# Optimization experiments

Measured on AMD Instinct MI355X. Metric: run time of the kernel, lower is better.

## Reference

```python
import jax, jax.numpy as jnp
import numpy as np

EPS = 1e-12


def setup_inputs() -> dict:
    key = jax.random.key(0)
    k1, k2, k3, k4 = jax.random.split(key, 4)
    N, H, W, D, K = 64, 32, 32, 512, 64
    x = jax.random.normal(k1, (N, H, W, D), dtype=jnp.float32)
    W_assign = jax.random.normal(k2, (D, K), dtype=jnp.float32) * 0.05  # 1x1 conv kernel
    b_assign = jax.random.normal(k3, (K,), dtype=jnp.float32) * 0.05
    C = jax.random.normal(k4, (D, K), dtype=jnp.float32) * 0.05  # cluster centers
    return {"x": x, "W_assign": W_assign, "b_assign": b_assign, "C": C}


def _l2norm(v, axis):
    return v / jnp.sqrt(jnp.sum(v * v, axis=axis, keepdims=True) + EPS)


def reference(x, W_assign, b_assign, C):
    # 1x1 conv = matmul over channel dim: [N,H,W,D] @ [D,K] -> [N,H,W,K]
    s = jnp.einsum('nhwd,dk->nhwk', x, W_assign) + b_assign
    a = jax.nn.softmax(s, axis=-1)                       # soft assignment over K
    # VLAD: v[n,d,k] = sum_hw a[n,h,w,k] * (x[n,h,w,d] + C[d,k])
    # reformulated as two small contractions (no [N,H,W,D,K] intermediate):
    v = jnp.einsum('nhwd,nhwk->ndk', x, a)               # feature-weighted sums
    a_sum = jnp.sum(a, axis=(1, 2))                      # [N,K]
    v = v + a_sum[:, None, :] * C[None, :, :]            # [N,D,K]
    # intra-normalization: L2 over D per cluster (after transpose to [N,K,D])
    v = _l2norm(jnp.transpose(v, (0, 2, 1)), axis=-1)    # [N,K,D]
    v = jnp.transpose(v, (0, 2, 1))                      # [N,D,K]
    # flatten and final L2 normalize -> [N, D*K]
    v = v.reshape(v.shape[0], -1)
    return _l2norm(v, axis=-1)
```

## Files before the change

kernel.cpp:

```cpp
#include <hip/hip_runtime.h>


#define EPSF 1e-12f

typedef short bf16x8 __attribute__((ext_vector_type(8)));
typedef float f32x16 __attribute__((ext_vector_type(16)));

__device__ inline unsigned short f2bf_rne(float f) {
  union { float f; unsigned u; } v; v.f = f;
  unsigned u = v.u;
  unsigned r = u + 0x7fffu + ((u >> 16) & 1u);
  return (unsigned short)(r >> 16);
}
__device__ inline unsigned pk2(float a, float b) {
#if __has_builtin(__builtin_amdgcn_cvt_pk_bf16_f32)
  auto r = __builtin_amdgcn_cvt_pk_bf16_f32(a, b);
  return __builtin_bit_cast(unsigned, r);
#else
  return (unsigned)f2bf_rne(a) | ((unsigned)f2bf_rne(b) << 16);
#endif
}

__global__ __launch_bounds__(256) void kprep(
    const float* __restrict__ Wm, unsigned short* __restrict__ wt) {
  __shared__ float tile[64][65];
  const int t = threadIdx.x, bx = blockIdx.x;
  {
    int col = (t & 15) * 4, rbase = t >> 4;
#pragma unroll
    for (int r = 0; r < 4; ++r) {
      int row = rbase + 16 * r;
      *(float4*)&tile[row][col] =
          *(const float4*)&Wm[(size_t)(bx * 64 + row) * 64 + col];
    }
  }
  __syncthreads();
  int k = t >> 2, seg = (t & 3) * 16;
  size_t o = (size_t)k * 512 + bx * 64 + seg;
#pragma unroll
  for (int j = 0; j < 16; j += 2)
    *(unsigned*)&wt[o + j] = pk2(tile[seg + j][k], tile[seg + j + 1][k]);
}

__global__ __launch_bounds__(256) void kassign(
    const float* __restrict__ x, const unsigned short* __restrict__ wt,
    const float* __restrict__ b, unsigned short* __restrict__ at,
    unsigned short* __restrict__ xt, float* __restrict__ a_sum) {
  __shared__ unsigned short xs[128][72];
  __shared__ unsigned short ws[64][72];
  const int t = threadIdx.x;
  const int w = t >> 6, lane = t & 63, l31 = lane & 31, h = lane >> 5;
  const int p0 = blockIdx.x * 128;
  const int n = p0 >> 10;
  const int hwbase = p0 & 1023;
  const int q8 = (t >> 4) * 8, c4 = (t & 15) * 4;
  const int wk = t >> 2, wseg = (t & 3) * 16;

  float4 px[8];
  uint4 pw0, pw1;
#pragma unroll
  for (int j = 0; j < 8; ++j)
    px[j] = *(const float4*)&x[(size_t)(p0 + q8 + j) * 512 + c4];
  pw0 = *(const uint4*)&wt[(size_t)wk * 512 + wseg];
  pw1 = *(const uint4*)&wt[(size_t)wk * 512 + wseg + 8];

  f32x16 acc0, acc1;
#pragma unroll
  for (int i = 0; i < 16; ++i) { acc0[i] = 0.f; acc1[i] = 0.f; }

  for (int c = 0; c < 8; ++c) {
    const int dc = c * 64;
    __syncthreads();
#pragma unroll
    for (int j = 0; j < 8; ++j) {
      uint2 ph;
      ph.x = pk2(px[j].x, px[j].y);
      ph.y = pk2(px[j].z, px[j].w);
      *(uint2*)&xs[q8 + j][c4] = ph;
    }
    *(uint4*)&ws[wk][wseg] = pw0;
    *(uint4*)&ws[wk][wseg + 8] = pw1;
    {
      const float* p = (const float*)px;
#pragma unroll
      for (int i = 0; i < 4; ++i) {
        uint4 o;
        o.x = pk2(px[0][i], px[1][i]);
        o.y = pk2(px[2][i], px[3][i]);
        o.z = pk2(px[4][i], px[5][i]);
        o.w = pk2(px[6][i], px[7][i]);
        *(uint4*)&xt[((size_t)n * 512 + dc + c4 + i) * 1024 + hwbase + q8] = o;
      }
      (void)p;
    }
    __syncthreads();
    if (c < 7) {
      const int dn = (c + 1) * 64;
#pragma unroll
      for (int j = 0; j < 8; ++j)
        px[j] = *(const float4*)&x[(size_t)(p0 + q8 + j) * 512 + dn + c4];
      pw0 = *(const uint4*)&wt[(size_t)wk * 512 + dn + wseg];
      pw1 = *(const uint4*)&wt[(size_t)wk * 512 + dn + wseg + 8];
    }
#pragma unroll
    for (int s = 0; s < 4; ++s) {
      int kd = s * 16 + h * 8;
      bf16x8 ax = *(const bf16x8*)&xs[32 * w + l31][kd];
      bf16x8 b0 = *(const bf16x8*)&ws[l31][kd];
      bf16x8 b1 = *(const bf16x8*)&ws[32 + l31][kd];
      acc0 = __builtin_amdgcn_mfma_f32_32x32x16_bf16(ax, b0, acc0, 0, 0, 0);
      acc1 = __builtin_amdgcn_mfma_f32_32x32x16_bf16(ax, b1, acc1, 0, 0, 0);
    }
  }

  const float bias0 = b[l31], bias1 = b[32 + l31];
  float a0[16], a1[16];
  float sum0 = 0.f, sum1 = 0.f;
#pragma unroll
  for (int r = 0; r < 16; ++r) {
    float s0 = acc0[r] + bias0, s1 = acc1[r] + bias1;
    float m = fmaxf(s0, s1);
#pragma unroll
    for (int msk = 1; msk < 32; msk <<= 1) m = fmaxf(m, __shfl_xor(m, msk, 64));
    float e0 = __expf(s0 - m), e1 = __expf(s1 - m);
    float S = e0 + e1;
#pragma unroll
    for (int msk = 1; msk < 32; msk <<= 1) S += __shfl_xor(S, msk, 64);
    float inv = 1.0f / S;
    a0[r] = e0 * inv; a1[r] = e1 * inv;
    sum0 += a0[r]; sum1 += a1[r];
  }
  const int hwb = hwbase + 32 * w + 4 * h;
  const size_t kb0 = ((size_t)n * 64 + l31) * 1024;
  const size_t kb1 = ((size_t)n * 64 + 32 + l31) * 1024;
#pragma unroll
  for (int g = 0; g < 4; ++g) {
    int hw = hwb + 8 * g;
    uint2 u;
    u.x = pk2(a0[4 * g + 0], a0[4 * g + 1]);
    u.y = pk2(a0[4 * g + 2], a0[4 * g + 3]);
    *(uint2*)&at[kb0 + hw] = u;
    u.x = pk2(a1[4 * g + 0], a1[4 * g + 1]);
    u.y = pk2(a1[4 * g + 2], a1[4 * g + 3]);
    *(uint2*)&at[kb1 + hw] = u;
  }
  sum0 += __shfl_xor(sum0, 32, 64);
  sum1 += __shfl_xor(sum1, 32, 64);
  if (lane < 32) {
    atomicAdd(&a_sum[n * 64 + l31], sum0);
    atomicAdd(&a_sum[n * 64 + 32 + l31], sum1);
  }
}

__global__ __launch_bounds__(256) void kvlad(
    const unsigned short* __restrict__ xt, const unsigned short* __restrict__ at,
    const float* __restrict__ a_sum, const float* __restrict__ C,
    float* __restrict__ out, float* __restrict__ ssq) {
  __shared__ unsigned short xa[64][72];
  __shared__ unsigned short as_[64][72];
  const int t = threadIdx.x;
  const int w = t >> 6, lane = t & 63, l31 = lane & 31, h = lane >> 5;
  const int n = blockIdx.y, d0 = blockIdx.x * 64;
  const int dw = 32 * (w & 1), kw = 32 * (w >> 1);
  const int sd = t >> 2, sseg = (t & 3) * 16;
  const size_t xbase = ((size_t)n * 512 + d0 + sd) * 1024;
  const size_t abase = ((size_t)n * 64 + sd) * 1024;

  uint4 px0, px1, pa0, pa1;
  px0 = *(const uint4*)&xt[xbase + sseg];
  px1 = *(const uint4*)&xt[xbase + sseg + 8];
  pa0 = *(const uint4*)&at[abase + sseg];
  pa1 = *(const uint4*)&at[abase + sseg + 8];

  f32x16 acc;
#pragma unroll
  for (int i = 0; i < 16; ++i) acc[i] = 0.f;

  for (int c = 0; c < 16; ++c) {
    __syncthreads();
    *(uint4*)&xa[sd][sseg] = px0;
    *(uint4*)&xa[sd][sseg + 8] = px1;
    *(uint4*)&as_[sd][sseg] = pa0;
    *(uint4*)&as_[sd][sseg + 8] = pa1;
    __syncthreads();
    if (c < 15) {
      const int hw0 = (c + 1) * 64;
      px0 = *(const uint4*)&xt[xbase + hw0 + sseg];
      px1 = *(const uint4*)&xt[xbase + hw0 + sseg + 8];
      pa0 = *(const uint4*)&at[abase + hw0 + sseg];
      pa1 = *(const uint4*)&at[abase + hw0 + sseg + 8];
    }
#pragma unroll
    for (int s = 0; s < 4; ++s) {
      int kk = s * 16 + h * 8;
      bf16x8 ax = *(const bf16x8*)&xa[dw + l31][kk];
      bf16x8 bb = *(const bf16x8*)&as_[kw + l31][kk];
      acc = __builtin_amdgcn_mfma_f32_32x32x16_bf16(ax, bb, acc, 0, 0, 0);
    }
  }

  const int k = kw + l31;
  const float as = a_sum[n * 64 + k];
  float sq = 0.f;
#pragma unroll
  for (int r = 0; r < 16; ++r) {
    int row = (r & 3) + 8 * (r >> 2) + 4 * h;
    int d = d0 + dw + row;
    float o = acc[r] + as * C[(size_t)d * 64 + k];
    out[((size_t)n * 512 + d) * 64 + k] = o;
    sq += o * o;
  }
  atomicAdd(&ssq[n * 64 + k], sq);
}

__global__ __launch_bounds__(256) void kscale(
    float* __restrict__ out, const float* __restrict__ ssq) {
  const int n = blockIdx.y, slice = blockIdx.x;
  const int t = threadIdx.x, k = t & 63, rg = t >> 6;
  __shared__ float sk[64];
  __shared__ float tot;
  if (t < 64) {
    float c = ssq[n * 64 + t];
    sk[t] = rsqrtf(c + EPSF);
    float contrib = c / (c + EPSF);
#pragma unroll
    for (int m = 32; m; m >>= 1) contrib += __shfl_xor(contrib, m, 64);
    if (t == 0) tot = rsqrtf(contrib + EPSF);
  }
  __syncthreads();
  const float scale = sk[k] * tot;
  float* vb = out + (size_t)n * 32768 + (size_t)slice * 4096;
#pragma unroll
  for (int r = rg; r < 64; r += 4) vb[r * 64 + k] *= scale;
}

extern "C" void kernel_launch(void* const* d_in, const int* in_sizes, int n_in,
                              void* d_out, int out_size, void* d_ws, size_t ws_size,
                              hipStream_t stream) {
  const float* x  = (const float*)d_in[0];
  const float* Wm = (const float*)d_in[1];
  const float* b  = (const float*)d_in[2];
  const float* C  = (const float*)d_in[3];
  float* out = (float*)d_out;

  unsigned short* at = (unsigned short*)d_ws;
  unsigned short* xt = at + (size_t)64 * 64 * 1024;
  unsigned short* wt = xt + (size_t)64 * 512 * 1024;
  float* a_sum = (float*)(wt + (size_t)64 * 512);
  float* ssq   = a_sum + 4096;

  hipMemsetAsync(a_sum, 0, 8192 * sizeof(float), stream);
  kprep<<<dim3(8), dim3(256), 0, stream>>>(Wm, wt);
  kassign<<<dim3(512), dim3(256), 0, stream>>>(x, wt, b, at, xt, a_sum);
  kvlad<<<dim3(8, 64), dim3(256), 0, stream>>>(xt, at, a_sum, C, out, ssq);
  kscale<<<dim3(8, 64), dim3(256), 0, stream>>>(out, ssq);
}
```

Before: 246.3 us.

## Fuse all stages into one cooperative kernel with grid-wide syncs

Replaces the memset and four separate kernel launches with a single cooperative persistent kernel of 512 blocks that runs weight prep plus a_sum/ssq zeroing, assignment, VLAD accumulation and scaling, separated by grid.sync(). The VLAD stage also widens its hw tile from 64 to 128 per iteration, which halves the number of block barriers. The aim is to remove launch overhead and per-kernel tail gaps. In exchange, all 512 blocks must be co-resident, grid-wide barriers add their own cost, and the larger VLAD tile increases register pressure.

```diff
diff --git a/kernel.cpp b/kernel.cpp
--- a/kernel.cpp
+++ b/kernel.cpp
@@ -1,7 +1,10 @@
 #include <hip/hip_runtime.h>
+#include <hip/hip_cooperative_groups.h>
 
 
 #define EPSF 1e-12f
+
+namespace cg = cooperative_groups;
 
 typedef short bf16x8 __attribute__((ext_vector_type(8)));
 typedef float f32x16 __attribute__((ext_vector_type(16)));
@@ -21,67 +24,73 @@
 #endif
 }
 
-__global__ __launch_bounds__(256) void kprep(
-    const float* __restrict__ Wm, unsigned short* __restrict__ wt) {
-  __shared__ float tile[64][65];
-  const int t = threadIdx.x, bx = blockIdx.x;
-  {
+__global__ __launch_bounds__(256, 2) void mega(
+    const float* __restrict__ x, const float* __restrict__ Wm,
+    const float* __restrict__ b, const float* __restrict__ C,
+    float* __restrict__ out,
+    unsigned short* __restrict__ at, unsigned short* __restrict__ xt,
+    unsigned short* __restrict__ wt, float* __restrict__ a_sum,
+    float* __restrict__ ssq) {
+  cg::grid_group grid = cg::this_grid();
+  __shared__ char smem[34816];
+  const int t = threadIdx.x;
+  const int bid = blockIdx.x;
+  const int w = t >> 6, lane = t & 63, l31 = lane & 31, h = lane >> 5;
+
+  if (bid < 8) {
+    float (*tile)[65] = (float(*)[65])smem;
     int col = (t & 15) * 4, rbase = t >> 4;
 #pragma unroll
     for (int r = 0; r < 4; ++r) {
       int row = rbase + 16 * r;
       *(float4*)&tile[row][col] =
-          *(const float4*)&Wm[(size_t)(bx * 64 + row) * 64 + col];
-    }
-  }
-  __syncthreads();
-  int k = t >> 2, seg = (t & 3) * 16;
-  size_t o = (size_t)k * 512 + bx * 64 + seg;
-#pragma unroll
-  for (int j = 0; j < 16; j += 2)
-    *(unsigned*)&wt[o + j] = pk2(tile[seg + j][k], tile[seg + j + 1][k]);
-}
-
-__global__ __launch_bounds__(256) void kassign(
-    const float* __restrict__ x, const unsigned short* __restrict__ wt,
-    const float* __restrict__ b, unsigned short* __restrict__ at,
-    unsigned short* __restrict__ xt, float* __restrict__ a_sum) {
-  __shared__ unsigned short xs[128][72];
-  __shared__ unsigned short ws[64][72];
-  const int t = threadIdx.x;
-  const int w = t >> 6, lane = t & 63, l31 = lane & 31, h = lane >> 5;
-  const int p0 = blockIdx.x * 128;
-  const int n = p0 >> 10;
-  const int hwbase = p0 & 1023;
-  const int q8 = (t >> 4) * 8, c4 = (t & 15) * 4;
-  const int wk = t >> 2, wseg = (t & 3) * 16;
-
-  float4 px[8];
-  uint4 pw0, pw1;
-#pragma unroll
-  for (int j = 0; j < 8; ++j)
-    px[j] = *(const float4*)&x[(size_t)(p0 + q8 + j) * 512 + c4];
-  pw0 = *(const uint4*)&wt[(size_t)wk * 512 + wseg];
-  pw1 = *(const uint4*)&wt[(size_t)wk * 512 + wseg + 8];
-
-  f32x16 acc0, acc1;
-#pragma unroll
-  for (int i = 0; i < 16; ++i) { acc0[i] = 0.f; acc1[i] = 0.f; }
-
-  for (int c = 0; c < 8; ++c) {
-    const int dc = c * 64;
+          *(const float4*)&Wm[(size_t)(bid * 64 + row) * 64 + col];
+    }
     __syncthreads();
-#pragma unroll
-    for (int j = 0; j < 8; ++j) {
-      uint2 ph;
-      ph.x = pk2(px[j].x, px[j].y);
-      ph.y = pk2(px[j].z, px[j].w);
-      *(uint2*)&xs[q8 + j][c4] = ph;
-    }
-    *(uint4*)&ws[wk][wseg] = pw0;
-    *(uint4*)&ws[wk][wseg + 8] = pw1;
-    {
-      const float* p = (const float*)px;
+    int k = t >> 2, seg = (t & 3) * 16;
+    size_t o = (size_t)k * 512 + bid * 64 + seg;
+#pragma unroll
+    for (int j = 0; j < 16; j += 2)
+      *(unsigned*)&wt[o + j] = pk2(tile[seg + j][k], tile[seg + j + 1][k]);
+  } else if (bid < 16) {
+    float4 z = {0.f, 0.f, 0.f, 0.f};
+    *(float4*)&a_sum[(size_t)(bid - 8) * 1024 + t * 4] = z;
+  }
+  grid.sync();
+
+  {
+    unsigned short (*xs)[72] = (unsigned short(*)[72])smem;
+    unsigned short (*ws)[72] = (unsigned short(*)[72])(smem + 128 * 72 * 2);
+    const int p0 = bid * 128;
+    const int n = p0 >> 10;
+    const int hwbase = p0 & 1023;
+    const int q8 = (t >> 4) * 8, c4 = (t & 15) * 4;
+    const int wk = t >> 2, wseg = (t & 3) * 16;
+
+    float4 px[8];
+    uint4 pw0, pw1;
+#pragma unroll
+    for (int j = 0; j < 8; ++j)
+      px[j] = *(const float4*)&x[(size_t)(p0 + q8 + j) * 512 + c4];
+    pw0 = *(const uint4*)&wt[(size_t)wk * 512 + wseg];
+    pw1 = *(const uint4*)&wt[(size_t)wk * 512 + wseg + 8];
+
+    f32x16 acc0, acc1;
+#pragma unroll
+    for (int i = 0; i < 16; ++i) { acc0[i] = 0.f; acc1[i] = 0.f; }
+
+    for (int c = 0; c < 8; ++c) {
+      const int dc = c * 64;
+      __syncthreads();
+#pragma unroll
+      for (int j = 0; j < 8; ++j) {
+        uint2 ph;
+        ph.x = pk2(px[j].x, px[j].y);
+        ph.y = pk2(px[j].z, px[j].w);
+        *(uint2*)&xs[q8 + j][c4] = ph;
+      }
+      *(uint4*)&ws[wk][wseg] = pw0;
+      *(uint4*)&ws[wk][wseg + 8] = pw1;
 #pragma unroll
       for (int i = 0; i < 4; ++i) {
         uint4 o;
@@ -91,147 +100,154 @@
         o.w = pk2(px[6][i], px[7][i]);
         *(uint4*)&xt[((size_t)n * 512 + dc + c4 + i) * 1024 + hwbase + q8] = o;
       }
-      (void)p;
+      __syncthreads();
+      if (c < 7) {
+        const int dn = (c + 1) * 64;
+#pragma unroll
+        for (int j = 0; j < 8; ++j)
+          px[j] = *(const float4*)&x[(size_t)(p0 + q8 + j) * 512 + dn + c4];
+        pw0 = *(const uint4*)&wt[(size_t)wk * 512 + dn + wseg];
+        pw1 = *(const uint4*)&wt[(size_t)wk * 512 + dn + wseg + 8];
+      }
+#pragma unroll
+      for (int s = 0; s < 4; ++s) {
+        int kd = s * 16 + h * 8;
+        bf16x8 ax = *(const bf16x8*)&xs[32 * w + l31][kd];
+        bf16x8 b0 = *(const bf16x8*)&ws[l31][kd];
+        bf16x8 b1 = *(const bf16x8*)&ws[32 + l31][kd];
+        acc0 = __builtin_amdgcn_mfma_f32_32x32x16_bf16(ax, b0, acc0, 0, 0, 0);
+        acc1 = __builtin_amdgcn_mfma_f32_32x32x16_bf16(ax, b1, acc1, 0, 0, 0);
+      }
+    }
+
+    const float bias0 = b[l31], bias1 = b[32 + l31];
+    float a0[16], a1[16];
+    float sum0 = 0.f, sum1 = 0.f;
+#pragma unroll
+    for (int r = 0; r < 16; ++r) {
+      float s0 = acc0[r] + bias0, s1 = acc1[r] + bias1;
+      float m = fmaxf(s0, s1);
+#pragma unroll
+      for (int msk = 1; msk < 32; msk <<= 1) m = fmaxf(m, __shfl_xor(m, msk, 64));
+      float e0 = __expf(s0 - m), e1 = __expf(s1 - m);
+      float S = e0 + e1;
+#pragma unroll
+      for (int msk = 1; msk < 32; msk <<= 1) S += __shfl_xor(S, msk, 64);
+      float inv = 1.0f / S;
+      a0[r] = e0 * inv; a1[r] = e1 * inv;
+      sum0 += a0[r]; sum1 += a1[r];
+    }
+    const int hwb = hwbase + 32 * w + 4 * h;
+    const size_t kb0 = ((size_t)n * 64 + l31) * 1024;
+    const size_t kb1 = ((size_t)n * 64 + 32 + l31) * 1024;
+#pragma unroll
+    for (int g = 0; g < 4; ++g) {
+      int hw = hwb + 8 * g;
+      uint2 u;
+      u.x = pk2(a0[4 * g + 0], a0[4 * g + 1]);
+      u.y = pk2(a0[4 * g + 2], a0[4 * g + 3]);
+      *(uint2*)&at[kb0 + hw] = u;
+      u.x = pk2(a1[4 * g + 0], a1[4 * g + 1]);
+      u.y = pk2(a1[4 * g + 2], a1[4 * g + 3]);
+      *(uint2*)&at[kb1 + hw] = u;
+    }
+    sum0 += __shfl_xor(sum0, 32, 64);
+    sum1 += __shfl_xor(sum1, 32, 64);
+    if (lane < 32) {
+      atomicAdd(&a_sum[n * 64 + l31], sum0);
+      atomicAdd(&a_sum[n * 64 + 32 + l31], sum1);
+    }
+  }
+  grid.sync();
+
+  {
+    unsigned short (*xa)[136] = (unsigned short(*)[136])smem;
+    unsigned short (*as_)[136] = (unsigned short(*)[136])(smem + 64 * 136 * 2);
+    const int n = bid >> 3, d0 = (bid & 7) * 64;
+    const int dw = 32 * (w & 1), kw = 32 * (w >> 1);
+    const int sd = t >> 2, sseg = (t & 3) * 32;
+    const size_t xbase = ((size_t)n * 512 + d0 + sd) * 1024;
+    const size_t abase = ((size_t)n * 64 + sd) * 1024;
+
+    uint4 px0, px1, px2, px3, pa0, pa1, pa2, pa3;
+    px0 = *(const uint4*)&xt[xbase + sseg];
+    px1 = *(const uint4*)&xt[xbase + sseg + 8];
+    px2 = *(const uint4*)&xt[xbase + sseg + 16];
+    px3 = *(const uint4*)&xt[xbase + sseg + 24];
+    pa0 = *(const uint4*)&at[abase + sseg];
+    pa1 = *(const uint4*)&at[abase + sseg + 8];
+    pa2 = *(const uint4*)&at[abase + sseg + 16];
+    pa3 = *(const uint4*)&at[abase + sseg + 24];
+
+    f32x16 acc;
+#pragma unroll
+    for (int i = 0; i < 16; ++i) acc[i] = 0.f;
+
+    for (int c = 0; c < 8; ++c) {
+      __syncthreads();
+      *(uint4*)&xa[sd][sseg] = px0;
+      *(uint4*)&xa[sd][sseg + 8] = px1;
+      *(uint4*)&xa[sd][sseg + 16] = px2;
+      *(uint4*)&xa[sd][sseg + 24] = px3;
+      *(uint4*)&as_[sd][sseg] = pa0;
+      *(uint4*)&as_[sd][sseg + 8] = pa1;
+      *(uint4*)&as_[sd][sseg + 16] = pa2;
+      *(uint4*)&as_[sd][sseg + 24] = pa3;
+      __syncthreads();
+      if (c < 7) {
+        const int hw0 = (c + 1) * 128;
+        px0 = *(const uint4*)&xt[xbase + hw0 + sseg];
+        px1 = *(const uint4*)&xt[xbase + hw0 + sseg + 8];
+        px2 = *(const uint4*)&xt[xbase + hw0 + sseg + 16];
+        px3 = *(const uint4*)&xt[xbase + hw0 + sseg + 24];
+        pa0 = *(const uint4*)&at[abase + hw0 + sseg];
+        pa1 = *(const uint4*)&at[abase + hw0 + sseg + 8];
+        pa2 = *(const uint4*)&at[abase + hw0 + sseg + 16];
+        pa3 = *(const uint4*)&at[abase + hw0 + sseg + 24];
+      }
+#pragma unroll
+      for (int s = 0; s < 8; ++s) {
+        int kk = s * 16 + h * 8;
+        bf16x8 ax = *(const bf16x8*)&xa[dw + l31][kk];
+        bf16x8 bb = *(const bf16x8*)&as_[kw + l31][kk];
+        acc = __builtin_amdgcn_mfma_f32_32x32x16_bf16(ax, bb, acc, 0, 0, 0);
+      }
+    }
+
+    const int k = kw + l31;
+    const float as = a_sum[n * 64 + k];
+    float sq = 0.f;
+#pragma unroll
+    for (int r = 0; r < 16; ++r) {
+      int row = (r & 3) + 8 * (r >> 2) + 4 * h;
+      int d = d0 + dw + row;
+      float o = acc[r] + as * C[(size_t)d * 64 + k];
+      out[((size_t)n * 512 + d) * 64 + k] = o;
+      sq += o * o;
+    }
+    atomicAdd(&ssq[n * 64 + k], sq);
+  }
+  grid.sync();
+
+  {
+    const int n = bid >> 3, slice = bid & 7;
+    const int k = t & 63, rg = t >> 6;
+    float* sk = (float*)smem;
+    float* tot = sk + 64;
+    if (t < 64) {
+      float c = ssq[n * 64 + t];
+      sk[t] = rsqrtf(c + EPSF);
+      float contrib = c / (c + EPSF);
+#pragma unroll
+      for (int m = 32; m; m >>= 1) contrib += __shfl_xor(contrib, m, 64);
+      if (t == 0) *tot = rsqrtf(contrib + EPSF);
     }
     __syncthreads();
-    if (c < 7) {
-      const int dn = (c + 1) * 64;
-#pragma unroll
-      for (int j = 0; j < 8; ++j)
-        px[j] = *(const float4*)&x[(size_t)(p0 + q8 + j) * 512 + dn + c4];
-      pw0 = *(const uint4*)&wt[(size_t)wk * 512 + dn + wseg];
-      pw1 = *(const uint4*)&wt[(size_t)wk * 512 + dn + wseg + 8];
-    }
-#pragma unroll
-    for (int s = 0; s < 4; ++s) {
-      int kd = s * 16 + h * 8;
-      bf16x8 ax = *(const bf16x8*)&xs[32 * w + l31][kd];
-      bf16x8 b0 = *(const bf16x8*)&ws[l31][kd];
-      bf16x8 b1 = *(const bf16x8*)&ws[32 + l31][kd];
-      acc0 = __builtin_amdgcn_mfma_f32_32x32x16_bf16(ax, b0, acc0, 0, 0, 0);
-      acc1 = __builtin_amdgcn_mfma_f32_32x32x16_bf16(ax, b1, acc1, 0, 0, 0);
-    }
-  }
-
-  const float bias0 = b[l31], bias1 = b[32 + l31];
-  float a0[16], a1[16];
-  float sum0 = 0.f, sum1 = 0.f;
-#pragma unroll
-  for (int r = 0; r < 16; ++r) {
-    float s0 = acc0[r] + bias0, s1 = acc1[r] + bias1;
-    float m = fmaxf(s0, s1);
-#pragma unroll
-    for (int msk = 1; msk < 32; msk <<= 1) m = fmaxf(m, __shfl_xor(m, msk, 64));
-    float e0 = __expf(s0 - m), e1 = __expf(s1 - m);
-    float S = e0 + e1;
-#pragma unroll
-    for (int msk = 1; msk < 32; msk <<= 1) S += __shfl_xor(S, msk, 64);
-    float inv = 1.0f / S;
-    a0[r] = e0 * inv; a1[r] = e1 * inv;
-    sum0 += a0[r]; sum1 += a1[r];
-  }
-  const int hwb = hwbase + 32 * w + 4 * h;
-  const size_t kb0 = ((size_t)n * 64 + l31) * 1024;
-  const size_t kb1 = ((size_t)n * 64 + 32 + l31) * 1024;
-#pragma unroll
-  for (int g = 0; g < 4; ++g) {
-    int hw = hwb + 8 * g;
-    uint2 u;
-    u.x = pk2(a0[4 * g + 0], a0[4 * g + 1]);
-    u.y = pk2(a0[4 * g + 2], a0[4 * g + 3]);
-    *(uint2*)&at[kb0 + hw] = u;
-    u.x = pk2(a1[4 * g + 0], a1[4 * g + 1]);
-    u.y = pk2(a1[4 * g + 2], a1[4 * g + 3]);
-    *(uint2*)&at[kb1 + hw] = u;
-  }
-  sum0 += __shfl_xor(sum0, 32, 64);
-  sum1 += __shfl_xor(sum1, 32, 64);
-  if (lane < 32) {
-    atomicAdd(&a_sum[n * 64 + l31], sum0);
-    atomicAdd(&a_sum[n * 64 + 32 + l31], sum1);
-  }
-}
-
-__global__ __launch_bounds__(256) void kvlad(
-    const unsigned short* __restrict__ xt, const unsigned short* __restrict__ at,
-    const float* __restrict__ a_sum, const float* __restrict__ C,
-    float* __restrict__ out, float* __restrict__ ssq) {
-  __shared__ unsigned short xa[64][72];
-  __shared__ unsigned short as_[64][72];
-  const int t = threadIdx.x;
-  const int w = t >> 6, lane = t & 63, l31 = lane & 31, h = lane >> 5;
-  const int n = blockIdx.y, d0 = blockIdx.x * 64;
-  const int dw = 32 * (w & 1), kw = 32 * (w >> 1);
-  const int sd = t >> 2, sseg = (t & 3) * 16;
-  const size_t xbase = ((size_t)n * 512 + d0 + sd) * 1024;
-  const size_t abase = ((size_t)n * 64 + sd) * 1024;
-
-  uint4 px0, px1, pa0, pa1;
-  px0 = *(const uint4*)&xt[xbase + sseg];
-  px1 = *(const uint4*)&xt[xbase + sseg + 8];
-  pa0 = *(const uint4*)&at[abase + sseg];
-  pa1 = *(const uint4*)&at[abase + sseg + 8];
-
-  f32x16 acc;
-#pragma unroll
-  for (int i = 0; i < 16; ++i) acc[i] = 0.f;
-
-  for (int c = 0; c < 16; ++c) {
-    __syncthreads();
-    *(uint4*)&xa[sd][sseg] = px0;
-    *(uint4*)&xa[sd][sseg + 8] = px1;
-    *(uint4*)&as_[sd][sseg] = pa0;
-    *(uint4*)&as_[sd][sseg + 8] = pa1;
-    __syncthreads();
-    if (c < 15) {
-      const int hw0 = (c + 1) * 64;
-      px0 = *(const uint4*)&xt[xbase + hw0 + sseg];
-      px1 = *(const uint4*)&xt[xbase + hw0 + sseg + 8];
-      pa0 = *(const uint4*)&at[abase + hw0 + sseg];
-      pa1 = *(const uint4*)&at[abase + hw0 + sseg + 8];
-    }
-#pragma unroll
-    for (int s = 0; s < 4; ++s) {
-      int kk = s * 16 + h * 8;
-      bf16x8 ax = *(const bf16x8*)&xa[dw + l31][kk];
-      bf16x8 bb = *(const bf16x8*)&as_[kw + l31][kk];
-      acc = __builtin_amdgcn_mfma_f32_32x32x16_bf16(ax, bb, acc, 0, 0, 0);
-    }
-  }
-
-  const int k = kw + l31;
-  const float as = a_sum[n * 64 + k];
-  float sq = 0.f;
-#pragma unroll
-  for (int r = 0; r < 16; ++r) {
-    int row = (r & 3) + 8 * (r >> 2) + 4 * h;
-    int d = d0 + dw + row;
-    float o = acc[r] + as * C[(size_t)d * 64 + k];
-    out[((size_t)n * 512 + d) * 64 + k] = o;
-    sq += o * o;
-  }
-  atomicAdd(&ssq[n * 64 + k], sq);
-}
-
-__global__ __launch_bounds__(256) void kscale(
-    float* __restrict__ out, const float* __restrict__ ssq) {
-  const int n = blockIdx.y, slice = blockIdx.x;
-  const int t = threadIdx.x, k = t & 63, rg = t >> 6;
-  __shared__ float sk[64];
-  __shared__ float tot;
-  if (t < 64) {
-    float c = ssq[n * 64 + t];
-    sk[t] = rsqrtf(c + EPSF);
-    float contrib = c / (c + EPSF);
-#pragma unroll
-    for (int m = 32; m; m >>= 1) contrib += __shfl_xor(contrib, m, 64);
-    if (t == 0) tot = rsqrtf(contrib + EPSF);
-  }
-  __syncthreads();
-  const float scale = sk[k] * tot;
-  float* vb = out + (size_t)n * 32768 + (size_t)slice * 4096;
-#pragma unroll
-  for (int r = rg; r < 64; r += 4) vb[r * 64 + k] *= scale;
+    const float scale = sk[k] * (*tot);
+    float* vb = out + (size_t)n * 32768 + (size_t)slice * 4096;
+#pragma unroll
+    for (int r = rg; r < 64; r += 4) vb[r * 64 + k] *= scale;
+  }
 }
 
 extern "C" void kernel_launch(void* const* d_in, const int* in_sizes, int n_in,
@@ -249,9 +265,7 @@
   float* a_sum = (float*)(wt + (size_t)64 * 512);
   float* ssq   = a_sum + 4096;
 
-  hipMemsetAsync(a_sum, 0, 8192 * sizeof(float), stream);
-  kprep<<<dim3(8), dim3(256), 0, stream>>>(Wm, wt);
-  kassign<<<dim3(512), dim3(256), 0, stream>>>(x, wt, b, at, xt, a_sum);
-  kvlad<<<dim3(8, 64), dim3(256), 0, stream>>>(xt, at, a_sum, C, out, ssq);
-  kscale<<<dim3(8, 64), dim3(256), 0, stream>>>(out, ssq);
-}
+  void* args[] = {(void*)&x, (void*)&Wm, (void*)&b, (void*)&C, (void*)&out,
+                  (void*)&at, (void*)&xt, (void*)&wt, (void*)&a_sum, (void*)&ssq};
+  hipLaunchCooperativeKernel((const void*)mega, dim3(512), dim3(256), args, 0, stream);
+}
```

Result: slower. 421.2 us (+71.0%).
